# Kernel optimization log

Measured on AMD Instinct MI355X. Metric: run time of the kernel, lower is better.

Reference implementation:

```python
import jax, jax.numpy as jnp
import numpy as np

N, E, D = 8192, 4096, 256
EDGE_DENSITY = 0.05  # ~410 nodes per hyperedge; guarantees no empty edge


def _layernorm(x, gamma, beta, eps=1e-5):
    mu = jnp.mean(x, axis=-1, keepdims=True)
    var = jnp.mean((x - mu) ** 2, axis=-1, keepdims=True)
    return (x - mu) * jax.lax.rsqrt(var + eps) * gamma + beta


def setup_inputs() -> dict:
    key = jax.random.key(0)
    k1, k2, k3 = jax.random.split(key, 3)
    node_embeddings = jax.random.normal(k1, (N, D), dtype=jnp.float32)
    # scale 1/sqrt(N) keeps two chained NxN matmuls per layer numerically sane
    target_martrix = jax.random.normal(k2, (N, N), dtype=jnp.float32) / np.float32(np.sqrt(N))
    hypergraph_matrix = (jax.random.uniform(k3, (N, E)) < EDGE_DENSITY).astype(jnp.float32)
    ln_gamma = jnp.ones((D,), jnp.float32)
    ln_beta = jnp.zeros((D,), jnp.float32)
    return {
        "node_embeddings": node_embeddings,
        "target_martrix": target_martrix,
        "hypergraph_matrix": hypergraph_matrix,
        "ln_gamma": ln_gamma,
        "ln_beta": ln_beta,
        "num_layers": 3,
    }


def reference(node_embeddings, target_martrix, hypergraph_matrix, ln_gamma, ln_beta, num_layers):
    # --- propagation: num_layers rounds of A @ x then A.T @ (.), residual + LN ---
    last = node_embeddings
    source = node_embeddings
    for _ in range(num_layers):
        t = target_martrix @ last            # [N, D]
        source = target_martrix.T @ t        # [N, D]  (pre-residual, pre-norm)
        last = _layernorm(source + node_embeddings, ln_gamma, ln_beta)
        # dropout p=0.35 is identity in eval mode
    # --- hyperedge masked-mean + global max (the torch per-edge python loop) ---
    # NOTE: torch loop uses `source_embedding` of the LAST layer (pre-norm).
    Hb = (hypergraph_matrix > 0).astype(source.dtype)   # [N, E]
    sums = Hb.T @ source                                 # [E, D] segment sums
    counts = jnp.sum(Hb, axis=0)[:, None]                # [E, 1] (all > 0 by construction)
    means = sums / counts                                # per-edge masked mean
    return jnp.max(means, axis=0)                        # [D]
```

## Files before the change

kernel.cpp:

```cpp
#include <hip/hip_runtime.h>


typedef __bf16 bf16;
typedef __bf16 bf16x8 __attribute__((ext_vector_type(8)));
typedef float f32x4 __attribute__((ext_vector_type(4)));

__device__ __forceinline__ void gld_lds16(const bf16* g, bf16* l) {
  __builtin_amdgcn_global_load_lds(
      (const __attribute__((address_space(1))) unsigned int*)g,
      (__attribute__((address_space(3))) unsigned int*)l, 16, 0, 0);
}

template <int BN>
__global__ __launch_bounds__(512) void gemm_bt(const bf16* __restrict__ A,
                                               const bf16* __restrict__ B,
                                               float* __restrict__ P,
                                               int N, int K, int Ks) {
  constexpr int BM = 256, BK = 64;
  constexpr int TM = 8, TN = BN / 64;
  constexpr int QA = BM / 64, QB = BN / 64;

  __shared__ __align__(16) bf16 As[2][BM * BK];
  __shared__ __align__(16) bf16 Bs[2][BN * BK];

  const int t = threadIdx.x, w = t >> 6, l = t & 63;
  const int srow = l >> 3;
  const int schunk = (l & 7) ^ srow;
  const int n0 = blockIdx.x * BN;
  const int kbase = blockIdx.z * Ks;

  const bf16* gA = A + (size_t)(w * 8 + srow) * K + kbase + schunk * 8;
  const bf16* gB = B + (size_t)(n0 + w * 8 + srow) * K + kbase + schunk * 8;

  auto stage = [&](int kk, int buf) {
    const size_t ko = (size_t)kk * BK;
#pragma unroll
    for (int q = 0; q < QA; ++q)
      gld_lds16(gA + (size_t)(q * 64) * K + ko,
                &As[buf][(q * 64 + w * 8) * BK]);
#pragma unroll
    for (int q = 0; q < QB; ++q)
      gld_lds16(gB + (size_t)(q * 64) * K + ko,
                &Bs[buf][(q * 64 + w * 8) * BK]);
  };

  const int lm = l & 15, kq = l >> 4;
  const int wm = (w >> 2) * 128;
  const int wn = (w & 3) * (TN * 16);

  f32x4 acc[TM][TN] = {};
  const int nk = Ks / BK;

  stage(0, 0);
  stage(1, 1);

  for (int kk = 0; kk < nk; ++kk) {
    const int buf = kk & 1;
    if (kk + 1 < nk)
      asm volatile("s_waitcnt vmcnt(8)" ::: "memory");
    else
      asm volatile("s_waitcnt vmcnt(0)" ::: "memory");
    asm volatile("s_barrier" ::: "memory");

#pragma unroll
    for (int ks = 0; ks < 2; ++ks) {
      bf16x8 af[TM], bfr[TN];
#pragma unroll
      for (int i = 0; i < TM; ++i) {
        const int r = wm + i * 16 + lm;
        const int c = ((ks * 4 + kq) ^ (r & 7)) * 8;
        af[i] = *(const bf16x8*)(&As[buf][r * BK + c]);
      }
#pragma unroll
      for (int j = 0; j < TN; ++j) {
        const int r = wn + j * 16 + lm;
        const int c = ((ks * 4 + kq) ^ (r & 7)) * 8;
        bfr[j] = *(const bf16x8*)(&Bs[buf][r * BK + c]);
      }
#pragma unroll
      for (int i = 0; i < TM; ++i)
#pragma unroll
        for (int j = 0; j < TN; ++j)
          acc[i][j] = __builtin_amdgcn_mfma_f32_16x16x32_bf16(af[i], bfr[j],
                                                              acc[i][j], 0, 0, 0);
    }
    asm volatile("s_barrier" ::: "memory");
    if (kk + 2 < nk) stage(kk + 2, buf);
  }

  float* Pz = P + (size_t)blockIdx.z * BM * N;
#pragma unroll
  for (int i = 0; i < TM; ++i) {
    const int mrow = wm + i * 16 + kq * 4;
#pragma unroll
    for (int j = 0; j < TN; ++j) {
      const int col = n0 + wn + j * 16 + lm;
#pragma unroll
      for (int r = 0; r < 4; ++r)
        Pz[(size_t)(mrow + r) * N + col] = acc[i][j][r];
    }
  }
}

template <int S>
__global__ __launch_bounds__(256) void reduceS_bf16(const float* __restrict__ P,
                                                    bf16* __restrict__ out,
                                                    size_t MN) {
  const size_t i4 = ((size_t)blockIdx.x * 256 + threadIdx.x) * 4;
  if (i4 >= MN) return;
  f32x4 a = *(const f32x4*)(P + i4);
#pragma unroll
  for (int z = 1; z < S; ++z) a = a + *(const f32x4*)(P + (size_t)z * MN + i4);
  bf16 o[4] = {(bf16)a[0], (bf16)a[1], (bf16)a[2], (bf16)a[3]};
  *(int2*)(out + i4) = *(const int2*)o;
}

__global__ __launch_bounds__(256) void transpose_conv(
    const float* __restrict__ src, int R, int C, bf16* __restrict__ cpy,
    bf16* __restrict__ trb, float* __restrict__ trf) {
  __shared__ float tile[64][65];
  const int t = threadIdx.x;
  const int col = t & 63, rb4 = t >> 6;
  const int r0 = blockIdx.y * 64, c0 = blockIdx.x * 64;
#pragma unroll
  for (int rr = 0; rr < 64; rr += 4) {
    const int row = rr + rb4;
    const float v = src[(size_t)(r0 + row) * C + c0 + col];
    tile[row][col] = v;
    if (cpy) cpy[(size_t)(r0 + row) * C + c0 + col] = (bf16)v;
  }
  __syncthreads();
#pragma unroll
  for (int rr = 0; rr < 64; rr += 4) {
    const int row = rr + rb4;
    const float v = tile[col][row];
    const size_t di = (size_t)(c0 + row) * R + r0 + col;
    if (trb) trb[di] = (bf16)v;
    if (trf) trf[di] = v;
  }
}

__global__ __launch_bounds__(256) void ln_kernel(const float* __restrict__ P,
                                                 const float* __restrict__ x0t,
                                                 const float* __restrict__ gamma,
                                                 const float* __restrict__ beta,
                                                 bf16* __restrict__ Xt) {
  constexpr size_t MN = (size_t)256 * 8192;
  const int tx = threadIdx.x;
  const int ty = threadIdx.y;
  const int i = blockIdx.x * 32 + tx;
  float vbuf[32];
  float s = 0.f, s2 = 0.f;
#pragma unroll
  for (int dd = 0; dd < 32; ++dd) {
    const int d = ty * 32 + dd;
    const size_t idx = (size_t)d * 8192 + i;
    float v = x0t[idx];
#pragma unroll
    for (int z = 0; z < 8; ++z) v += P[(size_t)z * MN + idx];
    vbuf[dd] = v;
    s += v;
    s2 += v * v;
  }
  __shared__ float S[8][32], Q[8][32];
  S[ty][tx] = s;
  Q[ty][tx] = s2;
  __syncthreads();
  __shared__ float MU[32], RS[32];
  if (ty == 0) {
    float a = 0.f, b = 0.f;
#pragma unroll
    for (int r = 0; r < 8; ++r) {
      a += S[r][tx];
      b += Q[r][tx];
    }
    const float mu = a * (1.0f / 256.0f);
    const float var = b * (1.0f / 256.0f) - mu * mu;
    MU[tx] = mu;
    RS[tx] = rsqrtf(var + 1e-5f);
  }
  __syncthreads();
  const float mu = MU[tx], rs = RS[tx];
#pragma unroll
  for (int dd = 0; dd < 32; ++dd) {
    const int d = ty * 32 + dd;
    const float y = (vbuf[dd] - mu) * rs * gamma[d] + beta[d];
    Xt[(size_t)d * 8192 + i] = (bf16)y;
  }
}

__global__ __launch_bounds__(256) void counts_kernel(const bf16* __restrict__ Htb,
                                                     float* __restrict__ invc) {
  const int e = blockIdx.x;
  const bf16* row = Htb + (size_t)e * 8192;
  float s = 0.f;
  for (int i = threadIdx.x; i < 8192; i += 256) s += (float)row[i];
  __shared__ float red[256];
  red[threadIdx.x] = s;
  __syncthreads();
  for (int k = 128; k > 0; k >>= 1) {
    if (threadIdx.x < k) red[threadIdx.x] += red[threadIdx.x + k];
    __syncthreads();
  }
  if (threadIdx.x == 0) invc[e] = 1.0f / red[0];
}

__global__ __launch_bounds__(256) void final_max(const float* __restrict__ P,
                                                 const float* __restrict__ invc,
                                                 float* __restrict__ out,
                                                 int S) {
  constexpr size_t MN = (size_t)256 * 4096;
  const int d = blockIdx.x;
  float m = -3.4e38f;
  for (int e = threadIdx.x; e < 4096; e += 256) {
    const size_t idx = (size_t)d * 4096 + e;
    float s = 0.f;
    for (int z = 0; z < S; ++z) s += P[z * MN + idx];
    m = fmaxf(m, s * invc[e]);
  }
  __shared__ float red[256];
  red[threadIdx.x] = m;
  __syncthreads();
  for (int k = 128; k > 0; k >>= 1) {
    if (threadIdx.x < k)
      red[threadIdx.x] = fmaxf(red[threadIdx.x], red[threadIdx.x + k]);
    __syncthreads();
  }
  if (threadIdx.x == 0) out[d] = red[0];
}

extern "C" void kernel_launch(void* const* d_in, const int* in_sizes, int n_in,
                              void* d_out, int out_size, void* d_ws,
                              size_t ws_size, hipStream_t stream) {
  const float* x0 = (const float*)d_in[0];
  const float* T = (const float*)d_in[1];
  const float* H = (const float*)d_in[2];
  const float* gamma = (const float*)d_in[3];
  const float* beta = (const float*)d_in[4];

  constexpr int Nn = 8192, E = 4096, D = 256, K = 8192;

  char* w = (char*)d_ws;
  size_t off = 0;
  auto carve = [&](size_t bytes) {
    char* p = w + off;
    off += (bytes + 255) & ~(size_t)255;
    return p;
  };
  bf16* Tb = (bf16*)carve((size_t)Nn * Nn * 2);
  bf16* Tt = (bf16*)carve((size_t)Nn * Nn * 2);
  bf16* Htb = (bf16*)carve((size_t)E * Nn * 2);
  float* x0t = (float*)carve((size_t)D * Nn * 4);
  bf16* Xt = (bf16*)carve((size_t)D * Nn * 2);
  bf16* tt = (bf16*)carve((size_t)D * Nn * 2);
  bf16* stb = (bf16*)carve((size_t)D * Nn * 2);
  float* invc = (float*)carve((size_t)E * 4);
  float* P = (float*)carve((size_t)8 * D * Nn * 4);

  if (off > ws_size) {
    hipMemsetAsync(d_out, 0, (size_t)out_size * 4, stream);
    return;
  }

  transpose_conv<<<dim3(128, 128), 256, 0, stream>>>(T, Nn, Nn, Tb, Tt, nullptr);
  transpose_conv<<<dim3(64, 128), 256, 0, stream>>>(H, Nn, E, nullptr, Htb, nullptr);
  transpose_conv<<<dim3(4, 128), 256, 0, stream>>>(x0, Nn, D, nullptr, Xt, x0t);
  counts_kernel<<<E, 256, 0, stream>>>(Htb, invc);

  const size_t MN = (size_t)D * Nn;
  for (int layer = 0; layer < 3; ++layer) {
    gemm_bt<256><<<dim3(32, 1, 8), 512, 0, stream>>>(Xt, Tb, P, Nn, K, K / 8);
    reduceS_bf16<8><<<(int)(MN / 1024), 256, 0, stream>>>(P, tt, MN);
    gemm_bt<256><<<dim3(32, 1, 8), 512, 0, stream>>>(tt, Tt, P, Nn, K, K / 8);
    if (layer < 2) {
      ln_kernel<<<dim3(256), dim3(32, 8), 0, stream>>>(P, x0t, gamma, beta, Xt);
    } else {
      reduceS_bf16<8><<<(int)(MN / 1024), 256, 0, stream>>>(P, stb, MN);
    }
  }

  gemm_bt<256><<<dim3(16, 1, 16), 512, 0, stream>>>(stb, Htb, P, E, K, K / 16);
  final_max<<<D, 256, 0, stream>>>(P, invc, (float*)d_out, 16);
}
```

Before: 1.114 ms.

## Pre-pack GEMM operands into swizzled 256x64 tiles for contiguous LDS loads

All bf16 GEMM operands (T, T^T, H^T, activations) are now written in a packed tile layout of 256 rows by 64 k, with the XOR swizzle already applied. Each k-step becomes one contiguous 32KB block per operand, so the global-to-LDS loads are fully linear instead of 64 strided row segments. The producer kernels (transpose, reduce, layernorm) now scatter their output into this layout, which may cost some write coalescing. Hyperedge counts are also computed directly from the fp32 H with column sums and atomics, so the counts pass no longer depends on the transposed copy.

```diff
diff --git a/kernel.cpp b/kernel.cpp
--- a/kernel.cpp
+++ b/kernel.cpp
@@ -4,6 +4,11 @@
 typedef __bf16 bf16;
 typedef __bf16 bf16x8 __attribute__((ext_vector_type(8)));
 typedef float f32x4 __attribute__((ext_vector_type(4)));
+
+__device__ __forceinline__ size_t packIdx(int n, int k, int Kch) {
+  return ((size_t)(n >> 8) * Kch + (k >> 6)) * 16384 + (size_t)(n & 255) * 64 +
+         ((((k >> 3) & 7) ^ (n & 7)) << 3) + (k & 7);
+}
 
 __device__ __forceinline__ void gld_lds16(const bf16* g, bf16* l) {
   __builtin_amdgcn_global_load_lds(
@@ -11,45 +16,38 @@
       (__attribute__((address_space(3))) unsigned int*)l, 16, 0, 0);
 }
 
-template <int BN>
-__global__ __launch_bounds__(512) void gemm_bt(const bf16* __restrict__ A,
-                                               const bf16* __restrict__ B,
-                                               float* __restrict__ P,
-                                               int N, int K, int Ks) {
-  constexpr int BM = 256, BK = 64;
-  constexpr int TM = 8, TN = BN / 64;
-  constexpr int QA = BM / 64, QB = BN / 64;
-
-  __shared__ __align__(16) bf16 As[2][BM * BK];
-  __shared__ __align__(16) bf16 Bs[2][BN * BK];
+__global__ __launch_bounds__(512) void gemm_packed(const bf16* __restrict__ Ap,
+                                                   const bf16* __restrict__ Bp,
+                                                   float* __restrict__ P,
+                                                   int N, int Kch, int Ks) {
+  constexpr int TM = 8, TN = 4;
+  __shared__ __align__(16) bf16 As[2][256 * 64];
+  __shared__ __align__(16) bf16 Bs[2][256 * 64];
 
   const int t = threadIdx.x, w = t >> 6, l = t & 63;
-  const int srow = l >> 3;
-  const int schunk = (l & 7) ^ srow;
-  const int n0 = blockIdx.x * BN;
-  const int kbase = blockIdx.z * Ks;
-
-  const bf16* gA = A + (size_t)(w * 8 + srow) * K + kbase + schunk * 8;
-  const bf16* gB = B + (size_t)(n0 + w * 8 + srow) * K + kbase + schunk * 8;
+  const int n0 = blockIdx.x * 256;
+  const int kb0 = (blockIdx.z * Ks) >> 6;
+
+  const bf16* pA = Ap + (size_t)kb0 * 16384 + w * 512 + l * 8;
+  const bf16* pB =
+      Bp + ((size_t)(n0 >> 8) * Kch + kb0) * 16384 + w * 512 + l * 8;
 
   auto stage = [&](int kk, int buf) {
-    const size_t ko = (size_t)kk * BK;
-#pragma unroll
-    for (int q = 0; q < QA; ++q)
-      gld_lds16(gA + (size_t)(q * 64) * K + ko,
-                &As[buf][(q * 64 + w * 8) * BK]);
-#pragma unroll
-    for (int q = 0; q < QB; ++q)
-      gld_lds16(gB + (size_t)(q * 64) * K + ko,
-                &Bs[buf][(q * 64 + w * 8) * BK]);
+    const size_t ko = (size_t)kk * 16384;
+#pragma unroll
+    for (int q = 0; q < 4; ++q)
+      gld_lds16(pA + ko + q * 4096, &As[buf][(q * 64 + w * 8) * 64]);
+#pragma unroll
+    for (int q = 0; q < 4; ++q)
+      gld_lds16(pB + ko + q * 4096, &Bs[buf][(q * 64 + w * 8) * 64]);
   };
 
   const int lm = l & 15, kq = l >> 4;
   const int wm = (w >> 2) * 128;
-  const int wn = (w & 3) * (TN * 16);
+  const int wn = (w & 3) * 64;
 
   f32x4 acc[TM][TN] = {};
-  const int nk = Ks / BK;
+  const int nk = Ks >> 6;
 
   stage(0, 0);
   stage(1, 1);
@@ -69,13 +67,13 @@
       for (int i = 0; i < TM; ++i) {
         const int r = wm + i * 16 + lm;
         const int c = ((ks * 4 + kq) ^ (r & 7)) * 8;
-        af[i] = *(const bf16x8*)(&As[buf][r * BK + c]);
+        af[i] = *(const bf16x8*)(&As[buf][r * 64 + c]);
       }
 #pragma unroll
       for (int j = 0; j < TN; ++j) {
         const int r = wn + j * 16 + lm;
         const int c = ((ks * 4 + kq) ^ (r & 7)) * 8;
-        bfr[j] = *(const bf16x8*)(&Bs[buf][r * BK + c]);
+        bfr[j] = *(const bf16x8*)(&Bs[buf][r * 64 + c]);
       }
 #pragma unroll
       for (int i = 0; i < TM; ++i)
@@ -88,7 +86,7 @@
     if (kk + 2 < nk) stage(kk + 2, buf);
   }
 
-  float* Pz = P + (size_t)blockIdx.z * BM * N;
+  float* Pz = P + (size_t)blockIdx.z * 256 * N;
 #pragma unroll
   for (int i = 0; i < TM; ++i) {
     const int mrow = wm + i * 16 + kq * 4;
@@ -103,7 +101,7 @@
 }
 
 template <int S>
-__global__ __launch_bounds__(256) void reduceS_bf16(const float* __restrict__ P,
+__global__ __launch_bounds__(256) void reduceS_pack(const float* __restrict__ P,
                                                     bf16* __restrict__ out,
                                                     size_t MN) {
   const size_t i4 = ((size_t)blockIdx.x * 256 + threadIdx.x) * 4;
@@ -112,31 +110,32 @@
 #pragma unroll
   for (int z = 1; z < S; ++z) a = a + *(const f32x4*)(P + (size_t)z * MN + i4);
   bf16 o[4] = {(bf16)a[0], (bf16)a[1], (bf16)a[2], (bf16)a[3]};
-  *(int2*)(out + i4) = *(const int2*)o;
+  const int d = (int)(i4 >> 13), k = (int)(i4 & 8191);
+  *(int2*)(out + packIdx(d, k, 128)) = *(const int2*)o;
 }
 
 __global__ __launch_bounds__(256) void transpose_conv(
-    const float* __restrict__ src, int R, int C, bf16* __restrict__ cpy,
-    bf16* __restrict__ trb, float* __restrict__ trf) {
+    const float* __restrict__ src, int R, int C, bf16* __restrict__ cpyP,
+    bf16* __restrict__ trbP, float* __restrict__ trf) {
   __shared__ float tile[64][65];
   const int t = threadIdx.x;
   const int col = t & 63, rb4 = t >> 6;
   const int r0 = blockIdx.y * 64, c0 = blockIdx.x * 64;
+  const int KchC = C >> 6, KchR = R >> 6;
 #pragma unroll
   for (int rr = 0; rr < 64; rr += 4) {
     const int row = rr + rb4;
     const float v = src[(size_t)(r0 + row) * C + c0 + col];
     tile[row][col] = v;
-    if (cpy) cpy[(size_t)(r0 + row) * C + c0 + col] = (bf16)v;
+    if (cpyP) cpyP[packIdx(r0 + row, c0 + col, KchC)] = (bf16)v;
   }
   __syncthreads();
 #pragma unroll
   for (int rr = 0; rr < 64; rr += 4) {
     const int row = rr + rb4;
     const float v = tile[col][row];
-    const size_t di = (size_t)(c0 + row) * R + r0 + col;
-    if (trb) trb[di] = (bf16)v;
-    if (trf) trf[di] = v;
+    if (trbP) trbP[packIdx(c0 + row, r0 + col, KchR)] = (bf16)v;
+    if (trf) trf[(size_t)(c0 + row) * R + r0 + col] = v;
   }
 }
 
@@ -185,24 +184,23 @@
   for (int dd = 0; dd < 32; ++dd) {
     const int d = ty * 32 + dd;
     const float y = (vbuf[dd] - mu) * rs * gamma[d] + beta[d];
-    Xt[(size_t)d * 8192 + i] = (bf16)y;
-  }
-}
-
-__global__ __launch_bounds__(256) void counts_kernel(const bf16* __restrict__ Htb,
+    Xt[packIdx(d, i, 128)] = (bf16)y;
+  }
+}
+
+__global__ __launch_bounds__(256) void counts_from_H(const float* __restrict__ H,
+                                                     float* __restrict__ cnt) {
+  const int e = blockIdx.x * 256 + threadIdx.x;
+  const int i0 = blockIdx.y * 1024;
+  float s = 0.f;
+  for (int i = i0; i < i0 + 1024; ++i) s += H[(size_t)i * 4096 + e];
+  atomicAdd(&cnt[e], s);
+}
+
+__global__ __launch_bounds__(256) void invert_kernel(const float* __restrict__ cnt,
                                                      float* __restrict__ invc) {
-  const int e = blockIdx.x;
-  const bf16* row = Htb + (size_t)e * 8192;
-  float s = 0.f;
-  for (int i = threadIdx.x; i < 8192; i += 256) s += (float)row[i];
-  __shared__ float red[256];
-  red[threadIdx.x] = s;
-  __syncthreads();
-  for (int k = 128; k > 0; k >>= 1) {
-    if (threadIdx.x < k) red[threadIdx.x] += red[threadIdx.x + k];
-    __syncthreads();
-  }
-  if (threadIdx.x == 0) invc[e] = 1.0f / red[0];
+  const int e = blockIdx.x * 256 + threadIdx.x;
+  invc[e] = 1.0f / cnt[e];
 }
 
 __global__ __launch_bounds__(256) void final_max(const float* __restrict__ P,
@@ -239,6 +237,7 @@
   const float* beta = (const float*)d_in[4];
 
   constexpr int Nn = 8192, E = 4096, D = 256, K = 8192;
+  constexpr int Kch = K / 64;
 
   char* w = (char*)d_ws;
   size_t off = 0;
@@ -254,6 +253,7 @@
   bf16* Xt = (bf16*)carve((size_t)D * Nn * 2);
   bf16* tt = (bf16*)carve((size_t)D * Nn * 2);
   bf16* stb = (bf16*)carve((size_t)D * Nn * 2);
+  float* cnt = (float*)carve((size_t)E * 4);
   float* invc = (float*)carve((size_t)E * 4);
   float* P = (float*)carve((size_t)8 * D * Nn * 4);
 
@@ -262,23 +262,25 @@
     return;
   }
 
+  hipMemsetAsync(cnt, 0, (size_t)E * 4, stream);
   transpose_conv<<<dim3(128, 128), 256, 0, stream>>>(T, Nn, Nn, Tb, Tt, nullptr);
   transpose_conv<<<dim3(64, 128), 256, 0, stream>>>(H, Nn, E, nullptr, Htb, nullptr);
   transpose_conv<<<dim3(4, 128), 256, 0, stream>>>(x0, Nn, D, nullptr, Xt, x0t);
-  counts_kernel<<<E, 256, 0, stream>>>(Htb, invc);
+  counts_from_H<<<dim3(16, 8), 256, 0, stream>>>(H, cnt);
+  invert_kernel<<<16, 256, 0, stream>>>(cnt, invc);
 
   const size_t MN = (size_t)D * Nn;
   for (int layer = 0; layer < 3; ++layer) {
-    gemm_bt<256><<<dim3(32, 1, 8), 512, 0, stream>>>(Xt, Tb, P, Nn, K, K / 8);
-    reduceS_bf16<8><<<(int)(MN / 1024), 256, 0, stream>>>(P, tt, MN);
-    gemm_bt<256><<<dim3(32, 1, 8), 512, 0, stream>>>(tt, Tt, P, Nn, K, K / 8);
+    gemm_packed<<<dim3(32, 1, 8), 512, 0, stream>>>(Xt, Tb, P, Nn, Kch, K / 8);
+    reduceS_pack<8><<<(int)(MN / 1024), 256, 0, stream>>>(P, tt, MN);
+    gemm_packed<<<dim3(32, 1, 8), 512, 0, stream>>>(tt, Tt, P, Nn, Kch, K / 8);
     if (layer < 2) {
       ln_kernel<<<dim3(256), dim3(32, 8), 0, stream>>>(P, x0t, gamma, beta, Xt);
     } else {
-      reduceS_bf16<8><<<(int)(MN / 1024), 256, 0, stream>>>(P, stb, MN);
-    }
-  }
-
-  gemm_bt<256><<<dim3(16, 1, 16), 512, 0, stream>>>(stb, Htb, P, E, K, K / 16);
+      reduceS_pack<8><<<(int)(MN / 1024), 256, 0, stream>>>(P, stb, MN);
+    }
+  }
+
+  gemm_packed<<<dim3(16, 1, 16), 512, 0, stream>>>(stb, Htb, P, E, Kch, K / 16);
   final_max<<<D, 256, 0, stream>>>(P, invc, (float*)d_out, 16);
 }
```

After: 1.138 ms. 2.2% more time.
